# Kernel optimization log

Measured on AMD Instinct MI355X. Metric: run time of the kernel, lower is better.

Reference implementation:

```python
import jax, jax.numpy as jnp
import numpy as np

N, C, H, W = 8, 32, 224, 224
TM = 4


def setup_inputs() -> dict:
    key = jax.random.key(0)
    k1, k2 = jax.random.split(key)
    inputs = jax.random.normal(k1, (N, C, H, W), dtype=jnp.float32)
    # learned per-(tm, channel) perspective params: identity + small perturbation
    ident = jnp.array([1, 0, 0, 0, 1, 0, 0, 0], dtype=jnp.float32)
    wt_pers = ident[None, None, :] + 0.05 * jax.random.normal(k2, (TM, C, 8), dtype=jnp.float32)
    return {"inputs": inputs, "wt_pers": wt_pers}


def _perspective_forward(inputs, wt_pers):
    # inputs: (N, C, H, W); wt_pers: (TM, C, 8)
    n, ch, h, w = inputs.shape
    tm = wt_pers.shape[0]
    dt = inputs.dtype

    # get_theta_matrix: append trailing identity param (eye(3).flatten()[8:] == [1.0])
    theta = jnp.concatenate([wt_pers, jnp.ones((tm, ch, 1), dt)], axis=-1)
    pers = theta.reshape(tm, ch, 3, 3)

    # generate_grids: torch.meshgrid(x(len W), y(len H), indexing='ij') -> (W, H), flatten,
    # matmul, then view as (3, H, W). Replicate exactly (flatten of (W,H) reshaped to (H,W)).
    xs = jnp.linspace(-1.0, 1.0, w).astype(dt)
    ys = jnp.linspace(-1.0, 1.0, h).astype(dt)
    xg, yg = jnp.meshgrid(xs, ys, indexing='ij')  # (W, H)
    grid = jnp.stack([xg.ravel(), yg.ravel(), jnp.ones(w * h, dt)], axis=0)  # (3, W*H)

    bg = jnp.einsum('tcij,jp->tcip', pers, grid).reshape(tm, ch, 3, h, w)
    omega = bg[:, :, 2]
    x_s = bg[:, :, 0] / omega
    y_s = bg[:, :, 1] / omega

    # interpolate (faithful, incl. the (max-1) scaling and the wb weight as written)
    max_x = float(w - 1)
    max_y = float(h - 1)
    x = 0.5 * ((x_s + 1.0) * (max_x - 1.0))
    y = 0.5 * ((y_s + 1.0) * (max_y - 1.0))
    x0 = jnp.floor(x).astype(jnp.int32)
    x1 = x0 + 1
    y0 = jnp.floor(y).astype(jnp.int32)
    y1 = y0 + 1
    x0 = jnp.clip(x0, 0, w - 1)
    x1 = jnp.clip(x1, 0, w - 1)
    y0 = jnp.clip(y0, 0, h - 1)
    y1 = jnp.clip(y1, 0, h - 1)

    cidx = jnp.arange(ch).reshape(1, ch, 1, 1)

    def gather(yy, xx):
        # fancy index: (N basic) x (tm,ch,H,W advanced) -> (N, tm, ch, H, W)
        return inputs[:, cidx, yy, xx]

    Ia = gather(y0, x0)
    Ib = gather(y1, x0)
    Ic = gather(y0, x1)
    Id = gather(y1, x1)

    x0f = x0.astype(dt); x1f = x1.astype(dt)
    y0f = y0.astype(dt); y1f = y1.astype(dt)
    wa = (x1f - x) * (y1f - y)
    wb = (x1f - x) * (y1f - y0f)  # source uses (y1 - y0) here, not (y - y0)
    wc = (x - x0f) * (y1f - y)
    wd = (x - x0f) * (y - y0f)

    out = wa * Ia + wb * Ib + wc * Ic + wd * Id  # (N, tm, ch, H, W)
    # original: cat over tm at dim -1 -> (N,C,H,W,tm); permute(0,1,4,2,3); flatten(1,2)
    return out.transpose(0, 2, 1, 3, 4).reshape(n, ch * tm, h, w)


def reference(inputs, wt_pers):
    return _perspective_forward(inputs, wt_pers)
```

## Files before the change

kernel.cpp:

```cpp
#include <hip/hip_runtime.h>

#define N_  8
#define C_  32
#define H_  224
#define W_  224
#define TM_ 4
#define TA  32
#define TB  32
#define NC  4

__global__ __launch_bounds__(256, 4) void persp_kernel(
    const float* __restrict__ inp,
    const float* __restrict__ wt,
    float* __restrict__ out)
{
    __shared__ float tile[NC][TA][TB + 1];

    const int tid = threadIdx.x;
    const int c   = blockIdx.y;
    const int ta  = blockIdx.x / (W_ / TB);
    const int tb  = blockIdx.x % (W_ / TB);
    const int a0  = ta * TA;
    const int b0  = tb * TB;

    const int a_off = tid & 31;
    const int bgrp  = tid >> 5;
    const int a     = a0 + a_off;

    const float step = 2.0f / 223.0f;
    const float hx   = -1.0f + (float)a * step;

    const int j4 = (tid & 7) * 4;
    const int iw = tid >> 3;

    const size_t plane   = (size_t)H_ * W_;
    const size_t istride = (size_t)C_ * plane;
    const size_t ostride = (size_t)(C_ * TM_) * plane;

    const float* ibase = inp + (size_t)c * plane;

    for (int t = 0; t < TM_; ++t) {
        const float* th = wt + ((size_t)t * C_ + c) * 8;
        const float t0 = th[0], t1 = th[1], t2 = th[2], t3 = th[3];
        const float t4 = th[4], t5 = th[5], t6 = th[6], t7 = th[7];

        int   iA[4], iB[4], iC[4], iD[4];
        float wa[4], wb[4], wc[4], wd[4];

#pragma unroll
        for (int p = 0; p < 4; ++p) {
            const int b = b0 + bgrp + 8 * p;
            const float hy = -1.0f + (float)b * step;

            const float w0 = t0 * hx + t1 * hy + t2;
            const float w1 = t3 * hx + t4 * hy + t5;
            const float w2 = t6 * hx + t7 * hy + 1.0f;

            const float xs = w0 / w2;
            const float ys = w1 / w2;

            const float x = 0.5f * ((xs + 1.0f) * 222.0f);
            const float y = 0.5f * ((ys + 1.0f) * 222.0f);

            int x0i = (int)floorf(x);
            int y0i = (int)floorf(y);
            int x1i = x0i + 1;
            int y1i = y0i + 1;
            x0i = min(max(x0i, 0), W_ - 1);
            x1i = min(max(x1i, 0), W_ - 1);
            y0i = min(max(y0i, 0), H_ - 1);
            y1i = min(max(y1i, 0), H_ - 1);

            const float x0f = (float)x0i, x1f = (float)x1i;
            const float y0f = (float)y0i, y1f = (float)y1i;

            wa[p] = (x1f - x) * (y1f - y);
            wb[p] = (x1f - x) * (y1f - y0f);
            wc[p] = (x - x0f) * (y1f - y);
            wd[p] = (x - x0f) * (y - y0f);

            iA[p] = y0i * W_ + x0i;
            iB[p] = y1i * W_ + x0i;
            iC[p] = y0i * W_ + x1i;
            iD[p] = y1i * W_ + x1i;
        }

#pragma unroll
        for (int nh = 0; nh < N_ / NC; ++nh) {
            float va[NC][4], vb[NC][4], vc[NC][4], vd[NC][4];
#pragma unroll
            for (int nn = 0; nn < NC; ++nn) {
                const float* ib = ibase + (size_t)(nh * NC + nn) * istride;
#pragma unroll
                for (int p = 0; p < 4; ++p) {
                    va[nn][p] = ib[iA[p]];
                    vb[nn][p] = ib[iB[p]];
                    vc[nn][p] = ib[iC[p]];
                    vd[nn][p] = ib[iD[p]];
                }
            }
#pragma unroll
            for (int nn = 0; nn < NC; ++nn) {
#pragma unroll
                for (int p = 0; p < 4; ++p) {
                    tile[nn][a_off][bgrp + 8 * p] =
                        wa[p] * va[nn][p] + wb[p] * vb[nn][p] +
                        wc[p] * vc[nn][p] + wd[p] * vd[nn][p];
                }
            }
            __syncthreads();

            float* ob = out + ((size_t)(c * TM_ + t)) * plane
                            + (size_t)(a0 + iw) * W_ + (b0 + j4);
#pragma unroll
            for (int nn = 0; nn < NC; ++nn) {
                const int n = nh * NC + nn;
                float4 v;
                v.x = tile[nn][iw][j4 + 0];
                v.y = tile[nn][iw][j4 + 1];
                v.z = tile[nn][iw][j4 + 2];
                v.w = tile[nn][iw][j4 + 3];
                *reinterpret_cast<float4*>(ob + (size_t)n * ostride) = v;
            }
            __syncthreads();
        }
    }
}

extern "C" void kernel_launch(void* const* d_in, const int* in_sizes, int n_in,
                              void* d_out, int out_size, void* d_ws, size_t ws_size,
                              hipStream_t stream) {
    const float* inp = (const float*)d_in[0];
    const float* wt  = (const float*)d_in[1];
    float* out = (float*)d_out;

    dim3 grid((H_ / TA) * (W_ / TB), C_);
    persp_kernel<<<grid, 256, 0, stream>>>(inp, wt, out);
}
```

Measured before the change: 327.2 us.

## Double-buffer LDS tile and prefetch next gathers before the barrier

Restructures the per-(tm, batch-half) loop into a software pipeline. It computes geometry for the next tm and issues the next batch of global gathers before the barrier, so those loads overlap with the LDS-to-global store phase. A second shared-memory tile buffer lets each iteration use one barrier instead of two, with a manual lgkmcnt wait before s_barrier. The cost is double the LDS footprint and more live registers, which may hurt occupancy or cause spills.

```diff
diff --git a/kernel.cpp b/kernel.cpp
--- a/kernel.cpp
+++ b/kernel.cpp
@@ -14,7 +14,7 @@
     const float* __restrict__ wt,
     float* __restrict__ out)
 {
-    __shared__ float tile[NC][TA][TB + 1];
+    __shared__ float tile[2][NC][TA][TB + 1];
 
     const int tid = threadIdx.x;
     const int c   = blockIdx.y;
@@ -25,10 +25,9 @@
 
     const int a_off = tid & 31;
     const int bgrp  = tid >> 5;
-    const int a     = a0 + a_off;
 
     const float step = 2.0f / 223.0f;
-    const float hx   = -1.0f + (float)a * step;
+    const float hx   = -1.0f + (float)(a0 + a_off) * step;
 
     const int j4 = (tid & 7) * 4;
     const int iw = tid >> 3;
@@ -39,92 +38,102 @@
 
     const float* ibase = inp + (size_t)c * plane;
 
-    for (int t = 0; t < TM_; ++t) {
-        const float* th = wt + ((size_t)t * C_ + c) * 8;
-        const float t0 = th[0], t1 = th[1], t2 = th[2], t3 = th[3];
-        const float t4 = th[4], t5 = th[5], t6 = th[6], t7 = th[7];
+    int   iA[4], iB[4], iC[4], iD[4];
+    float wa[4], wb[4], wc[4], wd[4];
 
-        int   iA[4], iB[4], iC[4], iD[4];
-        float wa[4], wb[4], wc[4], wd[4];
+#define GEOM(T)                                                            \
+    {                                                                      \
+        const float* th_ = wt + ((size_t)(T) * C_ + c) * 8;                \
+        const float t0 = th_[0], t1 = th_[1], t2 = th_[2], t3 = th_[3];    \
+        const float t4 = th_[4], t5 = th_[5], t6 = th_[6], t7 = th_[7];    \
+        _Pragma("unroll")                                                  \
+        for (int p = 0; p < 4; ++p) {                                      \
+            const int b = b0 + bgrp + 8 * p;                               \
+            const float hy = -1.0f + (float)b * step;                      \
+            const float w0 = t0 * hx + t1 * hy + t2;                       \
+            const float w1 = t3 * hx + t4 * hy + t5;                       \
+            const float w2 = t6 * hx + t7 * hy + 1.0f;                     \
+            const float xs = w0 / w2;                                      \
+            const float ys = w1 / w2;                                      \
+            const float x = 0.5f * ((xs + 1.0f) * 222.0f);                 \
+            const float y = 0.5f * ((ys + 1.0f) * 222.0f);                 \
+            int x0i = (int)floorf(x);                                      \
+            int y0i = (int)floorf(y);                                      \
+            int x1i = x0i + 1;                                             \
+            int y1i = y0i + 1;                                             \
+            x0i = min(max(x0i, 0), W_ - 1);                                \
+            x1i = min(max(x1i, 0), W_ - 1);                                \
+            y0i = min(max(y0i, 0), H_ - 1);                                \
+            y1i = min(max(y1i, 0), H_ - 1);                                \
+            const float x0f = (float)x0i, x1f = (float)x1i;                \
+            const float y0f = (float)y0i, y1f = (float)y1i;                \
+            wa[p] = (x1f - x) * (y1f - y);                                 \
+            wb[p] = (x1f - x) * (y1f - y0f);                               \
+            wc[p] = (x - x0f) * (y1f - y);                                 \
+            wd[p] = (x - x0f) * (y - y0f);                                 \
+            iA[p] = y0i * W_ + x0i;                                        \
+            iB[p] = y1i * W_ + x0i;                                        \
+            iC[p] = y0i * W_ + x1i;                                        \
+            iD[p] = y1i * W_ + x1i;                                        \
+        }                                                                  \
+    }
+
+    float ga[NC][4], gb[NC][4], gc[NC][4], gd[NC][4];
+
+#define ISSUE(NH)                                                          \
+    _Pragma("unroll")                                                      \
+    for (int nn = 0; nn < NC; ++nn) {                                      \
+        const float* ib = ibase + (size_t)((NH) * NC + nn) * istride;      \
+        _Pragma("unroll")                                                  \
+        for (int p = 0; p < 4; ++p) {                                      \
+            ga[nn][p] = ib[iA[p]];                                         \
+            gb[nn][p] = ib[iB[p]];                                         \
+            gc[nn][p] = ib[iC[p]];                                         \
+            gd[nn][p] = ib[iD[p]];                                         \
+        }                                                                  \
+    }
+
+    GEOM(0);
+    ISSUE(0);
 
 #pragma unroll
-        for (int p = 0; p < 4; ++p) {
-            const int b = b0 + bgrp + 8 * p;
-            const float hy = -1.0f + (float)b * step;
+    for (int iv = 0; iv < 2 * TM_; ++iv) {
+        const int t   = iv >> 1;
+        const int nh  = iv & 1;
+        const int buf = iv & 1;
 
-            const float w0 = t0 * hx + t1 * hy + t2;
-            const float w1 = t3 * hx + t4 * hy + t5;
-            const float w2 = t6 * hx + t7 * hy + 1.0f;
+#pragma unroll
+        for (int nn = 0; nn < NC; ++nn)
+#pragma unroll
+            for (int p = 0; p < 4; ++p)
+                tile[buf][nn][a_off][bgrp + 8 * p] =
+                    wa[p] * ga[nn][p] + wb[p] * gb[nn][p] +
+                    wc[p] * gc[nn][p] + wd[p] * gd[nn][p];
 
-            const float xs = w0 / w2;
-            const float ys = w1 / w2;
-
-            const float x = 0.5f * ((xs + 1.0f) * 222.0f);
-            const float y = 0.5f * ((ys + 1.0f) * 222.0f);
-
-            int x0i = (int)floorf(x);
-            int y0i = (int)floorf(y);
-            int x1i = x0i + 1;
-            int y1i = y0i + 1;
-            x0i = min(max(x0i, 0), W_ - 1);
-            x1i = min(max(x1i, 0), W_ - 1);
-            y0i = min(max(y0i, 0), H_ - 1);
-            y1i = min(max(y1i, 0), H_ - 1);
-
-            const float x0f = (float)x0i, x1f = (float)x1i;
-            const float y0f = (float)y0i, y1f = (float)y1i;
-
-            wa[p] = (x1f - x) * (y1f - y);
-            wb[p] = (x1f - x) * (y1f - y0f);
-            wc[p] = (x - x0f) * (y1f - y);
-            wd[p] = (x - x0f) * (y - y0f);
-
-            iA[p] = y0i * W_ + x0i;
-            iB[p] = y1i * W_ + x0i;
-            iC[p] = y0i * W_ + x1i;
-            iD[p] = y1i * W_ + x1i;
+        if (iv < 2 * TM_ - 1) {
+            if (nh == 1) GEOM(t + 1);
+            ISSUE((iv + 1) & 1);
         }
 
+        asm volatile("s_waitcnt lgkmcnt(0)" ::: "memory");
+        __builtin_amdgcn_s_barrier();
+        asm volatile("" ::: "memory");
+
+        float* ob = out + ((size_t)(c * TM_ + t)) * plane
+                        + (size_t)(a0 + iw) * W_ + (b0 + j4);
 #pragma unroll
-        for (int nh = 0; nh < N_ / NC; ++nh) {
-            float va[NC][4], vb[NC][4], vc[NC][4], vd[NC][4];
-#pragma unroll
-            for (int nn = 0; nn < NC; ++nn) {
-                const float* ib = ibase + (size_t)(nh * NC + nn) * istride;
-#pragma unroll
-                for (int p = 0; p < 4; ++p) {
-                    va[nn][p] = ib[iA[p]];
-                    vb[nn][p] = ib[iB[p]];
-                    vc[nn][p] = ib[iC[p]];
-                    vd[nn][p] = ib[iD[p]];
-                }
-            }
-#pragma unroll
-            for (int nn = 0; nn < NC; ++nn) {
-#pragma unroll
-                for (int p = 0; p < 4; ++p) {
-                    tile[nn][a_off][bgrp + 8 * p] =
-                        wa[p] * va[nn][p] + wb[p] * vb[nn][p] +
-                        wc[p] * vc[nn][p] + wd[p] * vd[nn][p];
-                }
-            }
-            __syncthreads();
-
-            float* ob = out + ((size_t)(c * TM_ + t)) * plane
-                            + (size_t)(a0 + iw) * W_ + (b0 + j4);
-#pragma unroll
-            for (int nn = 0; nn < NC; ++nn) {
-                const int n = nh * NC + nn;
-                float4 v;
-                v.x = tile[nn][iw][j4 + 0];
-                v.y = tile[nn][iw][j4 + 1];
-                v.z = tile[nn][iw][j4 + 2];
-                v.w = tile[nn][iw][j4 + 3];
-                *reinterpret_cast<float4*>(ob + (size_t)n * ostride) = v;
-            }
-            __syncthreads();
+        for (int nn = 0; nn < NC; ++nn) {
+            const int n = nh * NC + nn;
+            float4 v;
+            v.x = tile[buf][nn][iw][j4 + 0];
+            v.y = tile[buf][nn][iw][j4 + 1];
+            v.z = tile[buf][nn][iw][j4 + 2];
+            v.w = tile[buf][nn][iw][j4 + 3];
+            *reinterpret_cast<float4*>(ob + (size_t)n * ostride) = v;
         }
     }
+#undef GEOM
+#undef ISSUE
 }
 
 extern "C" void kernel_launch(void* const* d_in, const int* in_sizes, int n_in,
```

After: 332.2 us. Within noise of the previous version (+1.5%).
